# Kernel tuning notes

Hardware: AMD Instinct MI355X
Metric: run time of the kernel (lower is better)

The kernel has to match this reference:

```python
import jax, jax.numpy as jnp
import numpy as np
from jax import lax

N = 63        # fixed by ConvTranspose chain: 3->5->9->17->33->63
ML = 3        # smoother mid channels
KS = 7        # smoother kernel size
MID = 32      # hypernet mid channels
K_ITERS = 5   # outer solver iterations
B = 256


def _conv2d(x, w, pad):
    return lax.conv_general_dilated(x, w, (1, 1), [(pad, pad), (pad, pad)],
                                    dimension_numbers=('NCHW', 'OIHW', 'NCHW'))


def _batch_conv2d(x, kernels):
    # per-sample 3x3 stencil conv via grouped conv: x [B,1,m,m], kernels [B,1,3,3]
    b, _, m1, m2 = x.shape
    out = lax.conv_general_dilated(x.reshape(1, b, m1, m2), kernels, (1, 1),
                                   [(0, 0), (0, 0)],
                                   dimension_numbers=('NCHW', 'OIHW', 'NCHW'),
                                   feature_group_count=b)
    return out.reshape(b, 1, m1 - 2, m2 - 2)


def _conv_transpose2d(x, w, b, stride, padding):
    # torch ConvTranspose2d: w layout [in, out, k, k]
    k = w.shape[-1]
    w2 = jnp.flip(w, (-2, -1)).transpose(1, 0, 2, 3)  # [out, in, k, k]
    p = k - 1 - padding
    y = lax.conv_general_dilated(x, w2, (1, 1), [(p, p), (p, p)],
                                 lhs_dilation=(stride, stride),
                                 dimension_numbers=('NCHW', 'OIHW', 'NCHW'))
    return y + b[None, :, None, None]


def _pad_bc(x):
    # F.pad (1,0,1,0) with 0 then (0,1,0,1) with 1
    x = jnp.pad(x, ((0, 0), (0, 0), (1, 0), (1, 0)))
    return jnp.pad(x, ((0, 0), (0, 0), (0, 1), (0, 1)), constant_values=1.0)


def _gelu(x):
    return jax.nn.gelu(x, approximate=False)  # torch nn.GELU default is exact


def setup_inputs() -> dict:
    key = jax.random.key(0)
    ks = jax.random.split(key, 24)
    s = 0.02
    d = {}
    d['x'] = jax.random.normal(ks[0], (B, 1, N, N), jnp.float32)
    d['f'] = jax.random.normal(ks[1], (B, 1, N, N), jnp.float32)
    d['kernelA'] = jax.random.normal(ks[2], (B, 1, 3, 3), jnp.float32)
    # smoother hypernetwork (two Linear(9->100->mL*ks*ks) stacks)
    d['fc1_w1'] = jax.random.normal(ks[3], (9, 100), jnp.float32) * s
    d['fc1_b1'] = jnp.zeros((100,), jnp.float32)
    d['fc1_w2'] = jax.random.normal(ks[4], (100, ML * KS * KS), jnp.float32) * s
    d['fc1_b2'] = jnp.zeros((ML * KS * KS,), jnp.float32)
    d['fc2_w1'] = jax.random.normal(ks[5], (9, 100), jnp.float32) * s
    d['fc2_b1'] = jnp.zeros((100,), jnp.float32)
    d['fc2_w2'] = jax.random.normal(ks[6], (100, ML * KS * KS), jnp.float32) * s
    d['fc2_b2'] = jnp.zeros((ML * KS * KS,), jnp.float32)
    # CNNFNS meta: 5 ConvTranspose2d layers (torch weight layout [in,out,k,k])
    d['ct1_w'] = jax.random.normal(ks[7], (1, MID, 3, 3), jnp.float32) * s
    d['ct1_b'] = jnp.zeros((MID,), jnp.float32)
    d['ct2_w'] = jax.random.normal(ks[8], (MID, MID, 3, 3), jnp.float32) * s
    d['ct2_b'] = jnp.zeros((MID,), jnp.float32)
    d['ct3_w'] = jax.random.normal(ks[9], (MID, MID, 3, 3), jnp.float32) * s
    d['ct3_b'] = jnp.zeros((MID,), jnp.float32)
    d['ct4_w'] = jax.random.normal(ks[10], (MID, MID, 3, 3), jnp.float32) * s
    d['ct4_b'] = jnp.zeros((MID,), jnp.float32)
    d['ct5_w'] = jax.random.normal(ks[11], (MID, 2, 3, 3), jnp.float32) * s
    d['ct5_b'] = jnp.zeros((2,), jnp.float32)
    return d


def reference(x, f, kernelA,
              fc1_w1, fc1_b1, fc1_w2, fc1_b2,
              fc2_w1, fc2_b1, fc2_w2, fc2_b2,
              ct1_w, ct1_b, ct2_w, ct2_b, ct3_w, ct3_b, ct4_w, ct4_b, ct5_w, ct5_b):
    bsz = x.shape[0]

    # --- hypernet weights depend only on kernelA: hoist out of the K loop ---
    flatA = kernelA.reshape(bsz, 9)
    w1 = (_gelu(flatA @ fc1_w1 + fc1_b1) @ fc1_w2 + fc1_b2).reshape(bsz, ML, 1, KS, KS)
    w2 = (_gelu(flatA @ fc2_w1 + fc2_b1) @ fc2_w2 + fc2_b2).reshape(bsz, 1, ML, KS, KS)

    h = _gelu(_conv_transpose2d(kernelA, ct1_w, ct1_b, 2, 1))
    h = _gelu(_conv_transpose2d(h, ct2_w, ct2_b, 2, 1))
    h = _gelu(_conv_transpose2d(h, ct3_w, ct3_b, 2, 1))
    h = _gelu(_conv_transpose2d(h, ct4_w, ct4_b, 2, 1))
    h = _conv_transpose2d(h, ct5_w, ct5_b, 2, 2)          # [B,2,N,N]
    hw = h.reshape(bsz, 1, N, N, 2)                        # memory-reinterp view as in torch
    wc = lax.complex(hw[..., 0], hw[..., 1])               # [B,1,N,N] complex

    def residual(xc):
        return f - _batch_conv2d(_pad_bc(xc), kernelA)

    def smoother(xc):
        r = residual(xc)
        def per(r_i, a_i, b_i):
            t = _conv2d(r_i[None], a_i, KS // 2)           # [1,ML,N,N]
            return _conv2d(t, b_i, KS // 2)[0]             # [1,N,N]
        g2 = jax.vmap(per)(r, w1, w2)
        return xc + g2

    def h_correct(r):
        r_hat = jnp.fft.fft2(r, norm='ortho')
        out_ft = r_hat * wc
        # torch irfft2(s=(N,N)) trims last dim to N//2+1
        return jnp.fft.irfft2(out_ft[..., : N // 2 + 1], s=(N, N), norm='ortho')

    for _ in range(K_ITERS):
        x = smoother(x)
        x = x + h_correct(residual(x))
    r = residual(x)
    return jnp.linalg.norm(r) / bsz
```

## Files before the change

kernel.cpp:

```cpp
#include <hip/hip_runtime.h>
#include <math.h>

#define NB   256
#define ND   63
#define NN   3969

__device__ __forceinline__ float gelu_f(float v){
    return 0.5f * v * (1.0f + erff(v * 0.70710678118654752440f));
}

#define FMA4(A, W, S) { (A).x=fmaf((W).x,(S),(A).x); (A).y=fmaf((W).y,(S),(A).y); \
                        (A).z=fmaf((W).z,(S),(A).z); (A).w=fmaf((W).w,(S),(A).w); }

union F4  { float4 v;    float a[4];  };
union W16 { float4 v[4]; float a[16]; };

__device__ __forceinline__ float4 gelu4(const F4& x){
    float4 r;
    r.x = gelu_f(x.a[0]); r.y = gelu_f(x.a[1]);
    r.z = gelu_f(x.a[2]); r.w = gelu_f(x.a[3]);
    return r;
}

__device__ __forceinline__ int dec_base(int uc, int H){
    int h2 = H >> 1;
    return (uc < h2) ? 4*uc : (uc < H) ? 4*(uc - h2) + 1 : 2*H;
}

template<int SIN, int SOUT, int OST>
__device__ __forceinline__ void ct_quad_stage(const float* __restrict__ cin,
                                              float* __restrict__ cout,
                                              const float* __restrict__ wb,
                                              const float* __restrict__ bsv,
                                              int tid){
    const int H  = (SOUT - 1) >> 1;
    const int UX = H + 1;
    const int NU = UX * UX * 8;
    for (int u = tid; u < NU; u += 512){
        const int cell = u >> 3, q = u & 7;
        const int ucy = cell / UX, ucx = cell - ucy*UX;
        const int oy = dec_base(ucy, H), ox = dec_base(ucx, H);
        const bool vx = (ox + 2 <= 2*H), vy = (oy + 2 <= 2*H);
        int nky, kyA[2], iyA[2];
        if (oy & 1){ nky=2; kyA[0]=0; iyA[0]=(oy+1)>>1; kyA[1]=2; iyA[1]=(oy-1)>>1; }
        else       { nky=1; kyA[0]=1; iyA[0]=oy>>1; kyA[1]=1; iyA[1]=0; }
        int nkx, kxA[2], ixA[2];
        if (ox & 1){ nkx=2; kxA[0]=0; ixA[0]=(ox+1)>>1; kxA[1]=2; ixA[1]=(ox-1)>>1; }
        else       { nkx=1; kxA[0]=1; ixA[0]=ox>>1; kxA[1]=1; ixA[1]=0; }
        F4 a00, a01, a10, a11;
        a00.v = ((const float4*)bsv)[q]; a01.v = a00.v; a10.v = a00.v; a11.v = a00.v;
        for (int yi = 0; yi < nky; yi++)
        for (int xi = 0; xi < nkx; xi++){
            const float* wp  = wb + (kyA[yi]*3 + kxA[xi])*1024 + 4*q;
            const float* p00 = cin + (iyA[yi]*SIN + ixA[xi])*36;
            const float* p01 = p00 + 36;
            const float* p10 = p00 + SIN*36;
            const float* p11 = p10 + 36;
            #pragma unroll
            for (int g = 0; g < 8; g++){
                F4 i00, i01, i10, i11;
                i00.v = *(const float4*)(p00 + 4*g);
                i01.v = *(const float4*)(p01 + 4*g);
                i10.v = *(const float4*)(p10 + 4*g);
                i11.v = *(const float4*)(p11 + 4*g);
                #pragma unroll
                for (int cc = 0; cc < 4; cc++){
                    float4 w = *(const float4*)(wp + (4*g + cc)*32);
                    FMA4(a00.v, w, i00.a[cc]);
                    FMA4(a01.v, w, i01.a[cc]);
                    FMA4(a10.v, w, i10.a[cc]);
                    FMA4(a11.v, w, i11.a[cc]);
                }
            }
        }
        float4 g00 = gelu4(a00), g01 = gelu4(a01), g10 = gelu4(a10), g11 = gelu4(a11);
        size_t base = (size_t)(oy*SOUT + ox)*OST + 4*q;
        *(float4*)(cout + base) = g00;
        if (vx)        *(float4*)(cout + base + 2*(size_t)OST) = g01;
        if (vy)        *(float4*)(cout + base + 2*(size_t)SOUT*OST) = g10;
        if (vx && vy)  *(float4*)(cout + base + 2*(size_t)(SOUT+1)*OST) = g11;
    }
}

__global__ __launch_bounds__(512) void k_ct1234(const float* __restrict__ kA,
                                                const float* __restrict__ cw1,
                                                const float* __restrict__ cw2,
                                                const float* __restrict__ cw3,
                                                const float* __restrict__ cw4,
                                                const float* __restrict__ b1,
                                                const float* __restrict__ b2,
                                                const float* __restrict__ b3,
                                                const float* __restrict__ b4,
                                                float* __restrict__ c4out,
                                                float* __restrict__ acc){
    __shared__ __align__(16) float wbuf[9216];
    __shared__ __align__(16) float w1s[288];
    __shared__ __align__(16) float c1s[31*36];
    __shared__ __align__(16) float c2s[91*36];
    __shared__ __align__(16) float c3s[307*36];
    __shared__ float b1s[32], b2s[32], b3s[32], b4s[32];
    const int b = blockIdx.x, tid = threadIdx.x;
    if (b == 0 && tid == 0) acc[0] = 0.f;
    for (int i = tid; i < 9216; i += 512){
        int ci = i / 288, co = (i / 9) & 31, tap = i % 9;
        wbuf[tap*1024 + ci*32 + co] = cw2[i];
    }
    if (tid < 288) w1s[(tid % 9)*32 + tid/9] = cw1[tid];
    if (tid < 32){ b1s[tid]=b1[tid]; b2s[tid]=b2[tid]; b3s[tid]=b3[tid]; b4s[tid]=b4[tid]; }
    __syncthreads();
    if (tid < 200){
        int px = tid >> 3, q = tid & 7;
        int oy = px / 5, ox = px % 5;
        F4 a4; a4.v = ((const float4*)b1s)[q];
        int nky, kyA[2], iyA[2];
        if (oy & 1){ nky=2; kyA[0]=0; iyA[0]=(oy+1)/2; kyA[1]=2; iyA[1]=(oy-1)/2; }
        else       { nky=1; kyA[0]=1; iyA[0]=oy/2; kyA[1]=1; iyA[1]=0; }
        int nkx, kxA[2], ixA[2];
        if (ox & 1){ nkx=2; kxA[0]=0; ixA[0]=(ox+1)/2; kxA[1]=2; ixA[1]=(ox-1)/2; }
        else       { nkx=1; kxA[0]=1; ixA[0]=ox/2; kxA[1]=1; ixA[1]=0; }
        const float* ab = kA + b*9;
        for (int yi = 0; yi < nky; yi++)
        for (int xi = 0; xi < nkx; xi++){
            float v = ab[iyA[yi]*3 + ixA[xi]];
            float4 w = *(const float4*)(w1s + (kyA[yi]*3 + kxA[xi])*32 + 4*q);
            FMA4(a4.v, w, v);
        }
        *(float4*)(c1s + px*36 + 4*q) = gelu4(a4);
    }
    __syncthreads();
    ct_quad_stage<5, 9, 36>(c1s, c2s, wbuf, b2s, tid);
    __syncthreads();
    for (int i = tid; i < 9216; i += 512){
        int ci = i / 288, co = (i / 9) & 31, tap = i % 9;
        wbuf[tap*1024 + ci*32 + co] = cw3[i];
    }
    __syncthreads();
    ct_quad_stage<9, 17, 36>(c2s, c3s, wbuf, b3s, tid);
    __syncthreads();
    for (int i = tid; i < 9216; i += 512){
        int ci = i / 288, co = (i / 9) & 31, tap = i % 9;
        wbuf[tap*1024 + ci*32 + co] = cw4[i];
    }
    __syncthreads();
    ct_quad_stage<17, 33, 32>(c3s, c4out + (size_t)b*(1089*32), wbuf, b4s, tid);
}

__global__ __launch_bounds__(512) void k_solve(const float* __restrict__ x0g,
                                               const float* __restrict__ f,
                                               const float* __restrict__ kAg,
                                               const float* __restrict__ w1a, const float* __restrict__ b1a,
                                               const float* __restrict__ w2a, const float* __restrict__ b2a,
                                               const float* __restrict__ w1b, const float* __restrict__ b1b,
                                               const float* __restrict__ w2b, const float* __restrict__ b2b,
                                               const float* __restrict__ cw5,
                                               const float* __restrict__ b5,
                                               const float* __restrict__ c4g,
                                               float* __restrict__ accg){
    __shared__ __align__(16) float xs[63*68 + 8];
    __shared__ __align__(16) float U[8576];
    __shared__ __align__(16) float Fs_r[4096];
    __shared__ __align__(16) float Fs_i[4096];
    __shared__ __align__(16) float vcs[4096];
    __shared__ float ws5b[576];
    __shared__ float w1s[148], w2s[148], dvs[64], ds_r[32], ds_i[32], red[8], hs[100];
    const int b = blockIdx.x, tid = threadIdx.x;
    float* rs = U;
    float* tc = U + 4288;
    float*  rP  = U;
    const float4* rP4 = (const float4*)U;
    float2* TtC = (float2*)(U + 4096);
    float2* MC2 = (float2*)U;
    float4* CC4 = (float4*)(U + 4096);
    float* c5s = U;
    const float4* F4r = (const float4*)Fs_r;
    const float4* F4i = (const float4*)Fs_i;
    const float4* vc4s = (const float4*)vcs;
    const float* fg = f + (size_t)b*NN;
    float ka[9];
    #pragma unroll
    for (int i = 0; i < 9; i++) ka[i] = kAg[b*9 + i];

    for (int i = tid; i < 4096; i += 512){
        int r = i >> 6, c = i & 63;
        float vr = 0.f, vi = 0.f;
        if (r < 63 && c < 63){
            int m = (r * c) % 63;
            float ang = 6.283185307179586f * (float)m / 63.0f;
            vr = cosf(ang); vi = -sinf(ang);
        }
        Fs_r[i] = vr; Fs_i[i] = vi;
    }
    for (int i = tid; i < 576; i += 512){
        int ci = i / 18, co = (i / 9) & 1, tap = i % 9;
        ws5b[tap*64 + ci*2 + co] = cw5[i];
    }
    for (int i = tid; i < NN; i += 512) xs[(i/ND)*68 + (i%ND)] = x0g[(size_t)b*NN + i];
    if (tid < 100){
        float s = b1a[tid];
        #pragma unroll
        for (int i = 0; i < 9; i++) s = fmaf(ka[i], w1a[i*100 + tid], s);
        hs[tid] = gelu_f(s);
    }
    __syncthreads();
    if (tid < 147){
        float s = b2a[tid];
        for (int k = 0; k < 100; k++) s = fmaf(hs[k], w2a[k*147 + tid], s);
        w1s[tid] = s;
    }
    __syncthreads();
    if (tid < 100){
        float s = b1b[tid];
        #pragma unroll
        for (int i = 0; i < 9; i++) s = fmaf(ka[i], w1b[i*100 + tid], s);
        hs[tid] = gelu_f(s);
    }
    __syncthreads();
    if (tid < 147){
        float s = b2b[tid];
        for (int k = 0; k < 100; k++) s = fmaf(hs[k], w2b[k*147 + tid], s);
        w2s[tid] = s;
    }
    {
        const float* ib = c4g + (size_t)b * (1089*32);
        float bb0 = b5[0], bb1 = b5[1];
        for (int p = tid; p < NN; p += 512){
            int oy = p / ND, ox = p % ND;
            float a0 = bb0, a1 = bb1;
            int nky, kyA[2], iyA[2];
            if ((oy & 1) == 0){ nky=2; kyA[0]=0; iyA[0]=oy/2+1; kyA[1]=2; iyA[1]=oy/2; }
            else              { nky=1; kyA[0]=1; iyA[0]=(oy+1)/2; kyA[1]=1; iyA[1]=0; }
            int nkx, kxA[2], ixA[2];
            if ((ox & 1) == 0){ nkx=2; kxA[0]=0; ixA[0]=ox/2+1; kxA[1]=2; ixA[1]=ox/2; }
            else              { nkx=1; kxA[0]=1; ixA[0]=(ox+1)/2; kxA[1]=1; ixA[1]=0; }
            for (int yi = 0; yi < nky; yi++)
            for (int xi = 0; xi < nkx; xi++){
                const float* ip = ib + ((size_t)iyA[yi]*33 + ixA[xi])*32;
                const float* wp = ws5b + (kyA[yi]*3 + kxA[xi])*64;
                #pragma unroll
                for (int g = 0; g < 8; g++){
                    F4 iv; iv.v = *(const float4*)(ip + 4*g);
                    #pragma unroll
                    for (int q = 0; q < 4; q++){
                        int ci = 4*g + q;
                        a0 = fmaf(iv.a[q], wp[ci*2],   a0);
                        a1 = fmaf(iv.a[q], wp[ci*2+1], a1);
                    }
                }
            }
            c5s[p]      = a0;
            c5s[NN + p] = a1;
        }
    }
    __syncthreads();
    {
        const float sc = 1.0f / 3969.0f;
        float4* vout = (float4*)vcs;
        for (int i = tid; i < 1024; i += 512){
            int ky = i >> 5, ct2 = i & 31;
            float4 o;
            #pragma unroll
            for (int j = 0; j < 2; j++){
                int kx = 2*ct2 + j;
                float re = 0.f, im = 0.f;
                if (kx <= 31){ int o2 = 2*(ky*ND + kx); re = c5s[o2]*sc; im = c5s[o2+1]*sc; }
                else if (kx <= 62){
                    int sy = (ND - ky) % ND, sx = ND - kx;
                    int o2 = 2*(sy*ND + sx); re = c5s[o2]*sc; im = -c5s[o2+1]*sc;
                }
                if (j == 0){ o.x = re; o.y = im; } else { o.z = re; o.w = im; }
            }
            vout[i] = o;
        }
        if (tid < 32){
            float2 d = {0.f, 0.f};
            if (tid >= 1){
                int iA = (ND - tid) * ND, iB = tid * ND;
                d.x = (c5s[2*iA]     - c5s[2*iB])     * sc;
                d.y = (c5s[2*iA + 1] + c5s[2*iB + 1]) * sc;
            }
            ((float2*)dvs)[tid] = d;
        }
    }
    __syncthreads();

    const int kt = tid >> 4, cg = tid & 15;

    for (int it = 0; it < 5; it++){
        { float4 z = {0.f,0.f,0.f,0.f}; float4* U4 = (float4*)U;
          for (int i = tid; i < 2144; i += 512) U4[i] = z; }
        __syncthreads();
        for (int i = tid; i < NN; i += 512){
            int y = i / ND, xx = i % ND;
            float s = 0.f;
            #pragma unroll
            for (int dy = 0; dy < 3; dy++){
                int u = y + dy;
                #pragma unroll
                for (int dx = 0; dx < 3; dx++){
                    int v = xx + dx;
                    float p;
                    if (u == 64 || v == 64)    p = 1.0f;
                    else if (u == 0 || v == 0) p = 0.0f;
                    else                       p = xs[(u-1)*68 + (v-1)];
                    s = fmaf(p, ka[dy*3 + dx], s);
                }
            }
            rs[y*68 + 3 + xx] = fg[i] - s;
        }
        __syncthreads();
        const bool act = tid < 504;
        const int y0 = tid >> 3, x0c = 8*(tid & 7);
        float acc2[8] = {};
        for (int c = 0; c < 3; c++){
            if (act){
                float a1[8] = {};
                for (int dy = 0; dy < 7; dy++){
                    int ry = y0 + dy - 3;
                    if (ry < 0 || ry >= 63) continue;
                    W16 w16;
                    const float4* rp = (const float4*)(rs + ry*68 + x0c);
                    w16.v[0]=rp[0]; w16.v[1]=rp[1]; w16.v[2]=rp[2]; w16.v[3]=rp[3];
                    #pragma unroll
                    for (int dx = 0; dx < 7; dx++){
                        float wv = w1s[c*49 + dy*7 + dx];
                        #pragma unroll
                        for (int t = 0; t < 8; t++) a1[t] = fmaf(wv, w16.a[t+dx], a1[t]);
                    }
                }
                int nw = 63 - x0c; if (nw > 8) nw = 8;
                for (int t = 0; t < nw; t++) tc[y0*68 + 3 + x0c + t] = a1[t];
            }
            __syncthreads();
            if (act){
                for (int dy = 0; dy < 7; dy++){
                    int ry = y0 + dy - 3;
                    if (ry < 0 || ry >= 63) continue;
                    W16 w16;
                    const float4* tp = (const float4*)(tc + ry*68 + x0c);
                    w16.v[0]=tp[0]; w16.v[1]=tp[1]; w16.v[2]=tp[2]; w16.v[3]=tp[3];
                    #pragma unroll
                    for (int dx = 0; dx < 7; dx++){
                        float wv = w2s[c*49 + dy*7 + dx];
                        #pragma unroll
                        for (int t = 0; t < 8; t++) acc2[t] = fmaf(wv, w16.a[t+dx], acc2[t]);
                    }
                }
            }
            __syncthreads();
        }
        if (act){
            int nw = 63 - x0c; if (nw > 8) nw = 8;
            for (int t = 0; t < nw; t++) xs[y0*68 + x0c + t] += acc2[t];
        }
        __syncthreads();
        for (int i = tid; i < 4096; i += 512){
            int y = i >> 6, xx = i & 63;
            float val = 0.f;
            if (y < 63 && xx < 63){
                float s = 0.f;
                #pragma unroll
                for (int dy = 0; dy < 3; dy++){
                    int u = y + dy;
                    #pragma unroll
                    for (int dx = 0; dx < 3; dx++){
                        int v = xx + dx;
                        float p;
                        if (u == 64 || v == 64)    p = 1.0f;
                        else if (u == 0 || v == 0) p = 0.0f;
                        else                       p = xs[(u-1)*68 + (v-1)];
                        s = fmaf(p, ka[dy*3 + dx], s);
                    }
                }
                val = fg[y*ND + xx] - s;
            }
            rP[i] = val;
        }
        __syncthreads();
        {
            float tr0=0.f,ti0=0.f,tr1=0.f,ti1=0.f,tr2=0.f,ti2=0.f,tr3=0.f,ti3=0.f;
            for (int mq = 0; mq < 16; mq++){
                F4 f4r, f4i;
                f4r.v = F4r[kt*16 + mq];
                f4i.v = F4i[kt*16 + mq];
                #pragma unroll
                for (int j = 0; j < 4; j++){
                    F4 rv; rv.v = rP4[(4*mq + j)*16 + cg];
                    float fr = f4r.a[j], fi = f4i.a[j];
                    tr0 = fmaf(fr, rv.a[0], tr0); ti0 = fmaf(fi, rv.a[0], ti0);
                    tr1 = fmaf(fr, rv.a[1], tr1); ti1 = fmaf(fi, rv.a[1], ti1);
                    tr2 = fmaf(fr, rv.a[2], tr2); ti2 = fmaf(fi, rv.a[2], ti2);
                    tr3 = fmaf(fr, rv.a[3], tr3); ti3 = fmaf(fi, rv.a[3], ti3);
                }
            }
            const int c0 = 4*cg;
            TtC[(c0+0)*32 + ((kt + c0 + 0) & 31)] = make_float2(tr0, ti0);
            TtC[(c0+1)*32 + ((kt + c0 + 1) & 31)] = make_float2(tr1, ti1);
            TtC[(c0+2)*32 + ((kt + c0 + 2) & 31)] = make_float2(tr2, ti2);
            TtC[(c0+3)*32 + ((kt + c0 + 3) & 31)] = make_float2(tr3, ti3);
        }
        __syncthreads();
        {
            float R0r=0.f,R0i=0.f,R1r=0.f,R1i=0.f,R2r=0.f,R2i=0.f,R3r=0.f,R3i=0.f;
            for (int n = 0; n < 63; n++){
                float2 T = TtC[n*32 + ((kt + n) & 31)];
                F4 fr, fi;
                fr.v = F4r[n*16 + cg];
                fi.v = F4i[n*16 + cg];
                R0r = fmaf(T.x, fr.a[0], R0r); R0r = fmaf(-T.y, fi.a[0], R0r);
                R0i = fmaf(T.x, fi.a[0], R0i); R0i = fmaf( T.y, fr.a[0], R0i);
                R1r = fmaf(T.x, fr.a[1], R1r); R1r = fmaf(-T.y, fi.a[1], R1r);
                R1i = fmaf(T.x, fi.a[1], R1i); R1i = fmaf( T.y, fr.a[1], R1i);
                R2r = fmaf(T.x, fr.a[2], R2r); R2r = fmaf(-T.y, fi.a[2], R2r);
                R2i = fmaf(T.x, fi.a[2], R2i); R2i = fmaf( T.y, fr.a[2], R2i);
                R3r = fmaf(T.x, fr.a[3], R3r); R3r = fmaf(-T.y, fi.a[3], R3r);
                R3i = fmaf(T.x, fi.a[3], R3i); R3i = fmaf( T.y, fr.a[3], R3i);
            }
            if (cg == 0){
                float2 dv = ((const float2*)dvs)[kt];
                ds_r[kt] = R0r*dv.x + R0i*dv.y;
                ds_i[kt] = R0r*dv.y - R0i*dv.x;
            }
            float4 vA = vc4s[kt*32 + 2*cg];
            float4 vB = vc4s[kt*32 + 2*cg + 1];
            const int c0 = 4*cg, rot = kt;
            MC2[kt*64 + ((c0+0 + rot) & 63)] = make_float2(R0r*vA.x - R0i*vA.y, R0r*vA.y + R0i*vA.x);
            MC2[kt*64 + ((c0+1 + rot) & 63)] = make_float2(R1r*vA.z - R1i*vA.w, R1r*vA.w + R1i*vA.z);
            MC2[kt*64 + ((c0+2 + rot) & 63)] = make_float2(R2r*vB.x - R2i*vB.y, R2r*vB.y + R2i*vB.x);
            MC2[kt*64 + ((c0+3 + rot) & 63)] = make_float2(R3r*vB.z - R3i*vB.w, R3r*vB.w + R3i*vB.z);
        }
        __syncthreads();
        {
            float C0r=0.f,C0i=0.f,C1r=0.f,C1i=0.f,C2r=0.f,C2i=0.f,C3r=0.f,C3i=0.f;
            const int rot = kt;
            for (int l = 0; l < 63; l++){
                float2 Mv = MC2[kt*64 + ((l + rot) & 63)];
                F4 fr, fi;
                fr.v = F4r[l*16 + cg];
                fi.v = F4i[l*16 + cg];
                C0r = fmaf(Mv.x, fr.a[0], C0r); C0r = fmaf( Mv.y, fi.a[0], C0r);
                C0i = fmaf(Mv.y, fr.a[0], C0i); C0i = fmaf(-Mv.x, fi.a[0], C0i);
                C1r = fmaf(Mv.x, fr.a[1], C1r); C1r = fmaf( Mv.y, fi.a[1], C1r);
                C1i = fmaf(Mv.y, fr.a[1], C1i); C1i = fmaf(-Mv.x, fi.a[1], C1i);
                C2r = fmaf(Mv.x, fr.a[2], C2r); C2r = fmaf( Mv.y, fi.a[2], C2r);
                C2i = fmaf(Mv.y, fr.a[2], C2i); C2i = fmaf(-Mv.x, fi.a[2], C2i);
                C3r = fmaf(Mv.x, fr.a[3], C3r); C3r = fmaf( Mv.y, fi.a[3], C3r);
                C3i = fmaf(Mv.y, fr.a[3], C3i); C3i = fmaf(-Mv.x, fi.a[3], C3i);
            }
            float sc2 = (kt == 0) ? 0.5f : 1.0f;
            CC4[kt*33 + 2*cg]     = make_float4(C0r*sc2, C0i*sc2, C1r*sc2, C1i*sc2);
            CC4[kt*33 + 2*cg + 1] = make_float4(C2r*sc2, C2i*sc2, C3r*sc2, C3i*sc2);
        }
        __syncthreads();
        if (tid < 256){
            const int pr = tid >> 3, qb = tid & 7;
            float sr[8] = {}, si[8] = {};
            float er = 0.f, ei = 0.f;
            for (int nq = 0; nq < 8; nq++){
                F4 f4r, f4i;
                f4r.v = F4r[pr*16 + nq];
                f4i.v = F4i[pr*16 + nq];
                #pragma unroll
                for (int j = 0; j < 4; j++){
                    int n = 4*nq + j;
                    float fr = f4r.a[j], fi = f4i.a[j];
                    float4 cA = CC4[n*33 + qb];
                    float4 cB = CC4[n*33 + qb + 8];
                    float4 cC = CC4[n*33 + qb + 16];
                    float4 cD = CC4[n*33 + qb + 24];
                    sr[0]=fmaf(fr,cA.x,sr[0]); si[0]=fmaf(fi,cA.y,si[0]);
                    sr[1]=fmaf(fr,cA.z,sr[1]); si[1]=fmaf(fi,cA.w,si[1]);
                    sr[2]=fmaf(fr,cB.x,sr[2]); si[2]=fmaf(fi,cB.y,si[2]);
                    sr[3]=fmaf(fr,cB.z,sr[3]); si[3]=fmaf(fi,cB.w,si[3]);
                    sr[4]=fmaf(fr,cC.x,sr[4]); si[4]=fmaf(fi,cC.y,si[4]);
                    sr[5]=fmaf(fr,cC.z,sr[5]); si[5]=fmaf(fi,cC.w,si[5]);
                    sr[6]=fmaf(fr,cD.x,sr[6]); si[6]=fmaf(fi,cD.y,si[6]);
                    sr[7]=fmaf(fr,cD.z,sr[7]); si[7]=fmaf(fi,cD.w,si[7]);
                    er = fmaf(fr, ds_r[n], er); ei = fmaf(fi, ds_i[n], ei);
                }
            }
            {
                float e0 = er - ei;
                float* xrow = xs + pr*68;
                float2* xp0 = (float2*)(xrow + 2*qb);
                float2* xp1 = (float2*)(xrow + 2*qb + 16);
                float2* xp2 = (float2*)(xrow + 2*qb + 32);
                float2* xp3 = (float2*)(xrow + 2*qb + 48);
                float2 v0=*xp0, v1=*xp1, v2=*xp2, v3=*xp3;
                v0.x += 2.f*(sr[0]+si[0]) + e0; v0.y += 2.f*(sr[1]+si[1]) + e0;
                v1.x += 2.f*(sr[2]+si[2]) + e0; v1.y += 2.f*(sr[3]+si[3]) + e0;
                v2.x += 2.f*(sr[4]+si[4]) + e0; v2.y += 2.f*(sr[5]+si[5]) + e0;
                v3.x += 2.f*(sr[6]+si[6]) + e0; v3.y += 2.f*(sr[7]+si[7]) + e0;
                *xp0=v0; *xp1=v1; *xp2=v2; *xp3=v3;
            }
            if (pr > 0){
                float e1 = er + ei;
                float* xrow = xs + (63-pr)*68;
                float2* xp0 = (float2*)(xrow + 2*qb);
                float2* xp1 = (float2*)(xrow + 2*qb + 16);
                float2* xp2 = (float2*)(xrow + 2*qb + 32);
                float2* xp3 = (float2*)(xrow + 2*qb + 48);
                float2 v0=*xp0, v1=*xp1, v2=*xp2, v3=*xp3;
                v0.x += 2.f*(sr[0]-si[0]) + e1; v0.y += 2.f*(sr[1]-si[1]) + e1;
                v1.x += 2.f*(sr[2]-si[2]) + e1; v1.y += 2.f*(sr[3]-si[3]) + e1;
                v2.x += 2.f*(sr[4]-si[4]) + e1; v2.y += 2.f*(sr[5]-si[5]) + e1;
                v3.x += 2.f*(sr[6]-si[6]) + e1; v3.y += 2.f*(sr[7]-si[7]) + e1;
                *xp0=v0; *xp1=v1; *xp2=v2; *xp3=v3;
            }
        }
        __syncthreads();
    }
    float s = 0.f;
    for (int i = tid; i < NN; i += 512){
        int y = i / ND, xx = i % ND;
        float cv = 0.f;
        #pragma unroll
        for (int dy = 0; dy < 3; dy++){
            int u = y + dy;
            #pragma unroll
            for (int dx = 0; dx < 3; dx++){
                int v = xx + dx;
                float p;
                if (u == 64 || v == 64)    p = 1.0f;
                else if (u == 0 || v == 0) p = 0.0f;
                else                       p = xs[(u-1)*68 + (v-1)];
                cv = fmaf(p, ka[dy*3 + dx], cv);
            }
        }
        float r = fg[i] - cv;
        s = fmaf(r, r, s);
    }
    #pragma unroll
    for (int off = 32; off > 0; off >>= 1) s += __shfl_down(s, off, 64);
    int lane = tid & 63, w = tid >> 6;
    if (lane == 0) red[w] = s;
    __syncthreads();
    if (tid == 0){
        float t = 0.f;
        #pragma unroll
        for (int i = 0; i < 8; i++) t += red[i];
        atomicAdd(accg, t);
    }
}

__global__ void k_final(const float* __restrict__ acc, float* __restrict__ out){
    if (threadIdx.x == 0 && blockIdx.x == 0) out[0] = sqrtf(acc[0]) * (1.0f/256.0f);
}

extern "C" void kernel_launch(void* const* d_in, const int* in_sizes, int n_in,
                              void* d_out, int out_size, void* d_ws, size_t ws_size,
                              hipStream_t stream){
    const float* x0     = (const float*)d_in[0];
    const float* f      = (const float*)d_in[1];
    const float* kA     = (const float*)d_in[2];
    const float* fc1_w1 = (const float*)d_in[3];
    const float* fc1_b1 = (const float*)d_in[4];
    const float* fc1_w2 = (const float*)d_in[5];
    const float* fc1_b2 = (const float*)d_in[6];
    const float* fc2_w1 = (const float*)d_in[7];
    const float* fc2_b1 = (const float*)d_in[8];
    const float* fc2_w2 = (const float*)d_in[9];
    const float* fc2_b2 = (const float*)d_in[10];
    const float* ct1_w  = (const float*)d_in[11];
    const float* ct1_b  = (const float*)d_in[12];
    const float* ct2_w  = (const float*)d_in[13];
    const float* ct2_b  = (const float*)d_in[14];
    const float* ct3_w  = (const float*)d_in[15];
    const float* ct3_b  = (const float*)d_in[16];
    const float* ct4_w  = (const float*)d_in[17];
    const float* ct4_b  = (const float*)d_in[18];
    const float* ct5_w  = (const float*)d_in[19];
    const float* ct5_b  = (const float*)d_in[20];
    float* out = (float*)d_out;

    float* ws = (float*)d_ws;
    size_t off = 0;
    auto take = [&](size_t n){ float* p = ws + off; off += (n + 63) & ~(size_t)63; return p; };
    float* acc = take(64);
    float* c4  = take((size_t)NB*32*1089);
    (void)ws_size; (void)in_sizes; (void)n_in; (void)out_size;

    k_ct1234<<<NB, 512, 0, stream>>>(kA, ct1_w, ct2_w, ct3_w, ct4_w,
                                     ct1_b, ct2_b, ct3_b, ct4_b, c4, acc);
    k_solve<<<NB, 512, 0, stream>>>(x0, f, kA,
                                    fc1_w1, fc1_b1, fc1_w2, fc1_b2,
                                    fc2_w1, fc2_b1, fc2_w2, fc2_b2,
                                    ct5_w, ct5_b, c4, acc);
    k_final<<<1, 64, 0, stream>>>(acc, out);
}
```

Before: 398.6 us.

## Compute all three smoother channels in one pass with separate buffers

The first smoother conv now computes all three mid-channel outputs in one sweep over the residual and writes them to three separate shared buffers. The second conv then reads them without the per-channel barriers, cutting the smoother's syncs from six to two. The full zeroing of U is replaced by zeroing only the halo columns and tail of each buffer. The DFT twiddle tables are padded to a 68-float row stride (17 float4), apparently to spread LDS bank accesses. Shared memory per block grows substantially, which may reduce how many blocks fit per CU.

```diff
diff --git a/kernel.cpp b/kernel.cpp
--- a/kernel.cpp
+++ b/kernel.cpp
@@ -157,15 +157,17 @@
                                                const float* __restrict__ c4g,
                                                float* __restrict__ accg){
     __shared__ __align__(16) float xs[63*68 + 8];
-    __shared__ __align__(16) float U[8576];
-    __shared__ __align__(16) float Fs_r[4096];
-    __shared__ __align__(16) float Fs_i[4096];
+    __shared__ __align__(16) float U[17152 + 8];
+    __shared__ __align__(16) float Fs_r[4288];
+    __shared__ __align__(16) float Fs_i[4288];
     __shared__ __align__(16) float vcs[4096];
     __shared__ float ws5b[576];
     __shared__ float w1s[148], w2s[148], dvs[64], ds_r[32], ds_i[32], red[8], hs[100];
     const int b = blockIdx.x, tid = threadIdx.x;
-    float* rs = U;
-    float* tc = U + 4288;
+    float* rs  = U;
+    float* tc0 = U + 4288;
+    float* tc1 = U + 8576;
+    float* tc2 = U + 12864;
     float*  rP  = U;
     const float4* rP4 = (const float4*)U;
     float2* TtC = (float2*)(U + 4096);
@@ -180,8 +182,8 @@
     #pragma unroll
     for (int i = 0; i < 9; i++) ka[i] = kAg[b*9 + i];
 
-    for (int i = tid; i < 4096; i += 512){
-        int r = i >> 6, c = i & 63;
+    for (int i = tid; i < 4288; i += 512){
+        int r = i / 68, c = i % 68;
         float vr = 0.f, vi = 0.f;
         if (r < 63 && c < 63){
             int m = (r * c) % 63;
@@ -286,9 +288,6 @@
     const int kt = tid >> 4, cg = tid & 15;
 
     for (int it = 0; it < 5; it++){
-        { float4 z = {0.f,0.f,0.f,0.f}; float4* U4 = (float4*)U;
-          for (int i = tid; i < 2144; i += 512) U4[i] = z; }
-        __syncthreads();
         for (int i = tid; i < NN; i += 512){
             int y = i / ND, xx = i % ND;
             float s = 0.f;
@@ -307,36 +306,56 @@
             }
             rs[y*68 + 3 + xx] = fg[i] - s;
         }
+        for (int i = tid; i < 1276; i += 512){
+            int buf = i / 319, j = i - buf*319;
+            float* base = U + buf*4288;
+            int idx;
+            if (j < 315){ int rr = j/5, cc = j - rr*5; idx = rr*68 + ((cc < 3) ? cc : 63 + cc); }
+            else idx = 4284 + (j - 315);
+            base[idx] = 0.f;
+        }
         __syncthreads();
         const bool act = tid < 504;
         const int y0 = tid >> 3, x0c = 8*(tid & 7);
-        float acc2[8] = {};
-        for (int c = 0; c < 3; c++){
-            if (act){
-                float a1[8] = {};
+        if (act){
+            float A0[8] = {}, A1[8] = {}, A2[8] = {};
+            for (int dy = 0; dy < 7; dy++){
+                int ry = y0 + dy - 3;
+                if (ry < 0 || ry >= 63) continue;
+                W16 w16;
+                const float4* rp = (const float4*)(rs + ry*68 + x0c);
+                w16.v[0]=rp[0]; w16.v[1]=rp[1]; w16.v[2]=rp[2]; w16.v[3]=rp[3];
+                #pragma unroll
+                for (int dx = 0; dx < 7; dx++){
+                    float w0 = w1s[dy*7 + dx];
+                    float w1 = w1s[49 + dy*7 + dx];
+                    float w2 = w1s[98 + dy*7 + dx];
+                    #pragma unroll
+                    for (int t = 0; t < 8; t++){
+                        float v = w16.a[t+dx];
+                        A0[t] = fmaf(w0, v, A0[t]);
+                        A1[t] = fmaf(w1, v, A1[t]);
+                        A2[t] = fmaf(w2, v, A2[t]);
+                    }
+                }
+            }
+            int nw = 63 - x0c; if (nw > 8) nw = 8;
+            for (int t = 0; t < nw; t++){
+                int o = y0*68 + 3 + x0c + t;
+                tc0[o] = A0[t]; tc1[o] = A1[t]; tc2[o] = A2[t];
+            }
+        }
+        __syncthreads();
+        if (act){
+            float acc2[8] = {};
+            #pragma unroll
+            for (int c = 0; c < 3; c++){
+                const float* tcc = (c == 0) ? tc0 : (c == 1) ? tc1 : tc2;
                 for (int dy = 0; dy < 7; dy++){
                     int ry = y0 + dy - 3;
                     if (ry < 0 || ry >= 63) continue;
                     W16 w16;
-                    const float4* rp = (const float4*)(rs + ry*68 + x0c);
-                    w16.v[0]=rp[0]; w16.v[1]=rp[1]; w16.v[2]=rp[2]; w16.v[3]=rp[3];
-                    #pragma unroll
-                    for (int dx = 0; dx < 7; dx++){
-                        float wv = w1s[c*49 + dy*7 + dx];
-                        #pragma unroll
-                        for (int t = 0; t < 8; t++) a1[t] = fmaf(wv, w16.a[t+dx], a1[t]);
-                    }
-                }
-                int nw = 63 - x0c; if (nw > 8) nw = 8;
-                for (int t = 0; t < nw; t++) tc[y0*68 + 3 + x0c + t] = a1[t];
-            }
-            __syncthreads();
-            if (act){
-                for (int dy = 0; dy < 7; dy++){
-                    int ry = y0 + dy - 3;
-                    if (ry < 0 || ry >= 63) continue;
-                    W16 w16;
-                    const float4* tp = (const float4*)(tc + ry*68 + x0c);
+                    const float4* tp = (const float4*)(tcc + ry*68 + x0c);
                     w16.v[0]=tp[0]; w16.v[1]=tp[1]; w16.v[2]=tp[2]; w16.v[3]=tp[3];
                     #pragma unroll
                     for (int dx = 0; dx < 7; dx++){
@@ -346,9 +365,6 @@
                     }
                 }
             }
-            __syncthreads();
-        }
-        if (act){
             int nw = 63 - x0c; if (nw > 8) nw = 8;
             for (int t = 0; t < nw; t++) xs[y0*68 + x0c + t] += acc2[t];
         }
@@ -380,8 +396,8 @@
             float tr0=0.f,ti0=0.f,tr1=0.f,ti1=0.f,tr2=0.f,ti2=0.f,tr3=0.f,ti3=0.f;
             for (int mq = 0; mq < 16; mq++){
                 F4 f4r, f4i;
-                f4r.v = F4r[kt*16 + mq];
-                f4i.v = F4i[kt*16 + mq];
+                f4r.v = F4r[kt*17 + mq];
+                f4i.v = F4i[kt*17 + mq];
                 #pragma unroll
                 for (int j = 0; j < 4; j++){
                     F4 rv; rv.v = rP4[(4*mq + j)*16 + cg];
@@ -404,8 +420,8 @@
             for (int n = 0; n < 63; n++){
                 float2 T = TtC[n*32 + ((kt + n) & 31)];
                 F4 fr, fi;
-                fr.v = F4r[n*16 + cg];
-                fi.v = F4i[n*16 + cg];
+                fr.v = F4r[n*17 + cg];
+                fi.v = F4i[n*17 + cg];
                 R0r = fmaf(T.x, fr.a[0], R0r); R0r = fmaf(-T.y, fi.a[0], R0r);
                 R0i = fmaf(T.x, fi.a[0], R0i); R0i = fmaf( T.y, fr.a[0], R0i);
                 R1r = fmaf(T.x, fr.a[1], R1r); R1r = fmaf(-T.y, fi.a[1], R1r);
@@ -435,8 +451,8 @@
             for (int l = 0; l < 63; l++){
                 float2 Mv = MC2[kt*64 + ((l + rot) & 63)];
                 F4 fr, fi;
-                fr.v = F4r[l*16 + cg];
-                fi.v = F4i[l*16 + cg];
+                fr.v = F4r[l*17 + cg];
+                fi.v = F4i[l*17 + cg];
                 C0r = fmaf(Mv.x, fr.a[0], C0r); C0r = fmaf( Mv.y, fi.a[0], C0r);
                 C0i = fmaf(Mv.y, fr.a[0], C0i); C0i = fmaf(-Mv.x, fi.a[0], C0i);
                 C1r = fmaf(Mv.x, fr.a[1], C1r); C1r = fmaf( Mv.y, fi.a[1], C1r);
@@ -457,8 +473,8 @@
             float er = 0.f, ei = 0.f;
             for (int nq = 0; nq < 8; nq++){
                 F4 f4r, f4i;
-                f4r.v = F4r[pr*16 + nq];
-                f4i.v = F4i[pr*16 + nq];
+                f4r.v = F4r[pr*17 + nq];
+                f4i.v = F4i[pr*17 + nq];
                 #pragma unroll
                 for (int j = 0; j < 4; j++){
                     int n = 4*nq + j;
```

Result: faster. 373.7 us (-6.2%).
